# Kernel optimization log

Measured on AMD Instinct MI355X. Metric: run time of the kernel, lower is better.

## Reference

```python
import jax, jax.numpy as jnp
import numpy as np

IN_CHANNELS = 192
BAND_DIM = IN_CHANNELS // 3   # 64
HEADS = 4
HEAD_DIM = BAND_DIM // HEADS  # 16
SCALE = HEAD_DIM ** -0.5


def setup_inputs() -> dict:
    key = jax.random.key(0)
    k1, k2, k3 = jax.random.split(key, 3)
    B, H, W = 8, 128, 128
    hf = jax.random.normal(k1, (B, IN_CHANNELS, H, W), dtype=jnp.float32)
    # torch Linear weights, stored as (in, out) for direct matmul
    W_qkv = jax.random.normal(k2, (BAND_DIM, 3 * BAND_DIM), dtype=jnp.float32) * (BAND_DIM ** -0.5)
    W_proj = jax.random.normal(k3, (BAND_DIM, BAND_DIM), dtype=jnp.float32) * (BAND_DIM ** -0.5)
    b_proj = jnp.zeros((BAND_DIM,), dtype=jnp.float32)
    res_scale = jnp.float32(0.5)
    return {"hf": hf, "W_qkv": W_qkv, "W_proj": W_proj, "b_proj": b_proj, "res_scale": res_scale}


def reference(hf, W_qkv, W_proj, b_proj, res_scale):
    B, Ctot, H, W = hf.shape
    bd, h, hd = BAND_DIM, HEADS, HEAD_DIM
    # (B, 3, bd, H, W) -> (B, H, W, 3, bd) -> (N, 3, bd)
    x = hf.reshape(B, 3, bd, H, W).transpose(0, 3, 4, 1, 2).reshape(-1, 3, bd)
    qkv = x @ W_qkv                                   # (N, 3, 3*bd)
    q, k, v = jnp.split(qkv, 3, axis=-1)
    # (N, 3, bd) -> (N, heads, 3, hd)
    def split_heads(t):
        return t.reshape(-1, 3, h, hd).transpose(0, 2, 1, 3)
    q, k, v = split_heads(q), split_heads(k), split_heads(v)
    attn = jnp.einsum('nhqd,nhkd->nhqk', q, k) * SCALE  # (N, heads, 3, 3)
    attn = jax.nn.softmax(attn, axis=-1)
    y = jnp.einsum('nhqk,nhkd->nhqd', attn, v)          # (N, heads, 3, hd)
    y = y.transpose(0, 2, 1, 3).reshape(-1, 3, bd)      # (N, 3, bd)
    y = y @ W_proj + b_proj
    # (N, 3, bd) -> (B, H, W, 3, bd) -> (B, Ctot, H, W)
    y = y.reshape(B, H, W, 3, bd).transpose(0, 3, 4, 1, 2).reshape(B, Ctot, H, W)
    return hf + res_scale * y
```

## Files before the change

### kernel.cpp

```cpp
#include <hip/hip_runtime.h>


typedef __attribute__((ext_vector_type(8))) short bf16x8;
typedef __attribute__((ext_vector_type(4))) float f32x4;

constexpr int kHW = 16384;
constexpr int kC = 192;

__device__ __forceinline__ unsigned short f2bf(float f) {
  unsigned int u = __float_as_uint(f);
  return (unsigned short)((u + 0x7fffu + ((u >> 16) & 1u)) >> 16);
}

__global__ void pack_weights(const float* __restrict__ Wqkv,
                             const float* __restrict__ Wproj,
                             unsigned char* __restrict__ wsc) {
  const int tid = threadIdx.x;
  const int wid = tid >> 6;
  const int l = tid & 63;
  const int c = l & 15;
  const int g = l >> 4;
  for (int f = wid; f < 24; f += 4) {
    const int m = f >> 1, s = f & 1;
    const int row = m * 16 + c;
    const int k0 = s * 32 + g * 8;
    bf16x8 wf;
#pragma unroll
    for (int j = 0; j < 8; ++j) wf[j] = (short)f2bf(Wqkv[(k0 + j) * 192 + row]);
    *(bf16x8*)(wsc + f * 1024 + l * 16) = wf;
  }
  for (int f = wid; f < 8; f += 4) {
    const int m = f >> 1, s = f & 1;
    const int row = m * 16 + c;
    const int k0 = s * 32 + g * 8;
    bf16x8 wf;
#pragma unroll
    for (int j = 0; j < 8; ++j) wf[j] = (short)f2bf(Wproj[(k0 + j) * 64 + row]);
    *(bf16x8*)(wsc + 24576 + f * 1024 + l * 16) = wf;
  }
}

__global__ __launch_bounds__(256, 4) void hfattn_mfma2(
    const float* __restrict__ hf,
    const unsigned char* __restrict__ wfr,
    const float* __restrict__ bproj,
    const float* __restrict__ rscale,
    float* __restrict__ out) {
  __shared__ char smem[24576];

  const int tid = threadIdx.x;
  const int wid = tid >> 6;
  const int l = tid & 63;
  const int c = l & 15;
  const int g = l >> 4;

  char* const yBase = smem + wid * 6144;
  const f32x4 zz = {0.f, 0.f, 0.f, 0.f};

  const int pxB = blockIdx.x * 64 + wid * 16;
  const int b8 = pxB >> 14;
  const int blkBase = b8 * (kC * kHW);
  const int hw = (pxB & (kHW - 1)) + c;

  float bias_[4][4];
#pragma unroll
  for (int m = 0; m < 4; ++m)
#pragma unroll
    for (int j = 0; j < 4; ++j) bias_[m][j] = bproj[m * 16 + g * 4 + j];
  const float rv = rscale[0];

  bf16x8 Xf[3][2];
#pragma unroll
  for (int b = 0; b < 3; ++b)
#pragma unroll
    for (int s = 0; s < 2; ++s) {
      const int ch0 = b * 64 + s * 32 + g * 8;
      float xr[8];
#pragma unroll
      for (int j = 0; j < 8; ++j) xr[j] = hf[blkBase + (ch0 + j) * kHW + hw];
      bf16x8 xf;
#pragma unroll
      for (int j = 0; j < 8; ++j) xf[j] = (short)f2bf(xr[j]);
      Xf[b][s] = xf;
    }

#pragma unroll 1
  for (int h = 0; h < 4; ++h) {
    const bf16x8 qA0 = *(const bf16x8*)(wfr + (h * 2 + 0) * 1024 + l * 16);
    const bf16x8 qA1 = *(const bf16x8*)(wfr + (h * 2 + 1) * 1024 + l * 16);
    const bf16x8 kA0 = *(const bf16x8*)(wfr + ((4 + h) * 2 + 0) * 1024 + l * 16);
    const bf16x8 kA1 = *(const bf16x8*)(wfr + ((4 + h) * 2 + 1) * 1024 + l * 16);
    f32x4 q[3], k[3];
#pragma unroll
    for (int b = 0; b < 3; ++b) {
      q[b] = __builtin_amdgcn_mfma_f32_16x16x32_bf16(qA0, Xf[b][0], zz, 0, 0, 0);
      q[b] = __builtin_amdgcn_mfma_f32_16x16x32_bf16(qA1, Xf[b][1], q[b], 0, 0, 0);
      k[b] = __builtin_amdgcn_mfma_f32_16x16x32_bf16(kA0, Xf[b][0], zz, 0, 0, 0);
      k[b] = __builtin_amdgcn_mfma_f32_16x16x32_bf16(kA1, Xf[b][1], k[b], 0, 0, 0);
    }
    float P[3][3];
#pragma unroll
    for (int r1 = 0; r1 < 3; ++r1) {
      float sc[3];
#pragma unroll
      for (int r2 = 0; r2 < 3; ++r2) {
        float d = q[r1][0] * k[r2][0] + q[r1][1] * k[r2][1] +
                  q[r1][2] * k[r2][2] + q[r1][3] * k[r2][3];
        d += __shfl_xor(d, 16);
        d += __shfl_xor(d, 32);
        sc[r2] = d * 0.25f;
      }
      const float mx = fmaxf(sc[0], fmaxf(sc[1], sc[2]));
      const float e0 = __expf(sc[0] - mx);
      const float e1 = __expf(sc[1] - mx);
      const float e2 = __expf(sc[2] - mx);
      const float inv = 1.f / (e0 + e1 + e2);
      P[r1][0] = e0 * inv;
      P[r1][1] = e1 * inv;
      P[r1][2] = e2 * inv;
    }
    const bf16x8 vA0 = *(const bf16x8*)(wfr + ((8 + h) * 2 + 0) * 1024 + l * 16);
    const bf16x8 vA1 = *(const bf16x8*)(wfr + ((8 + h) * 2 + 1) * 1024 + l * 16);
    f32x4 v[3];
#pragma unroll
    for (int b = 0; b < 3; ++b) {
      v[b] = __builtin_amdgcn_mfma_f32_16x16x32_bf16(vA0, Xf[b][0], zz, 0, 0, 0);
      v[b] = __builtin_amdgcn_mfma_f32_16x16x32_bf16(vA1, Xf[b][1], v[b], 0, 0, 0);
    }
    const int sp = h >> 1;
    const int gp = (h & 1) * 2 + (g >> 1);
    const int wslot = (gp * 16 + c) * 16 + (g & 1) * 8;
#pragma unroll
    for (int r1 = 0; r1 < 3; ++r1) {
      float y0 = P[r1][0] * v[0][0] + P[r1][1] * v[1][0] + P[r1][2] * v[2][0];
      float y1 = P[r1][0] * v[0][1] + P[r1][1] * v[1][1] + P[r1][2] * v[2][1];
      float y2 = P[r1][0] * v[0][2] + P[r1][1] * v[1][2] + P[r1][2] * v[2][2];
      float y3 = P[r1][0] * v[0][3] + P[r1][1] * v[1][3] + P[r1][2] * v[2][3];
      uint2 pk;
      pk.x = (unsigned)f2bf(y0) | ((unsigned)f2bf(y1) << 16);
      pk.y = (unsigned)f2bf(y2) | ((unsigned)f2bf(y3) << 16);
      *(uint2*)(yBase + (r1 * 2 + sp) * 1024 + wslot) = pk;
    }
  }

#pragma unroll
  for (int b = 0; b < 3; ++b) {
    const bf16x8 yB0 = *(bf16x8*)(yBase + (b * 2 + 0) * 1024 + l * 16);
    const bf16x8 yB1 = *(bf16x8*)(yBase + (b * 2 + 1) * 1024 + l * 16);
#pragma unroll
    for (int m = 0; m < 4; ++m) {
      const bf16x8 pA0 =
          *(const bf16x8*)(wfr + 24576 + (m * 2 + 0) * 1024 + l * 16);
      const bf16x8 pA1 =
          *(const bf16x8*)(wfr + 24576 + (m * 2 + 1) * 1024 + l * 16);
      f32x4 o = __builtin_amdgcn_mfma_f32_16x16x32_bf16(pA0, yB0, zz, 0, 0, 0);
      o = __builtin_amdgcn_mfma_f32_16x16x32_bf16(pA1, yB1, o, 0, 0, 0);
#pragma unroll
      for (int j = 0; j < 4; ++j) {
        const int ch = b * 64 + m * 16 + g * 4 + j;
        const int a = blkBase + ch * kHW + hw;
        out[a] = hf[a] + rv * (o[j] + bias_[m][j]);
      }
    }
  }
}

extern "C" void kernel_launch(void* const* d_in, const int* in_sizes, int n_in,
                              void* d_out, int out_size, void* d_ws,
                              size_t ws_size, hipStream_t stream) {
  const float* hf = (const float*)d_in[0];
  const float* Wqkv = (const float*)d_in[1];
  const float* Wproj = (const float*)d_in[2];
  const float* bproj = (const float*)d_in[3];
  const float* rscale = (const float*)d_in[4];
  float* out = (float*)d_out;
  unsigned char* wsc = (unsigned char*)d_ws;

  hipLaunchKernelGGL(pack_weights, dim3(1), dim3(256), 0, stream, Wqkv, Wproj,
                     wsc);

  const int npix = in_sizes[0] / kC;
  const int nblocks = npix / 64;
  hipLaunchKernelGGL(hfattn_mfma2, dim3(nblocks), dim3(256), 0, stream, hf, wsc,
                     bproj, rscale, out);
}
```

Before: 60.40 us.

## Replace LDS staging of attention output with cross-lane shuffles and unroll heads

The attention output is no longer staged in shared memory. The per-head outputs are moved into the projection MFMA B-operand layout using wave shuffles, and the head loop is fully unrolled through templates with sched barriers. The residual hf reads are batched ahead of the projection MFMAs, and the bias is loaded as float4. This removes the LDS round-trip and 24KB of shared memory per block, which could raise occupancy. In exchange it adds many shuffle instructions and more register pressure from the unrolled heads.

```diff
diff --git a/kernel.cpp b/kernel.cpp
--- a/kernel.cpp
+++ b/kernel.cpp
@@ -40,33 +40,109 @@
   }
 }
 
-__global__ __launch_bounds__(256, 4) void hfattn_mfma2(
+template <int H>
+__device__ __forceinline__ void head_compute(const bf16x8* __restrict__ wp,
+                                             int l, const bf16x8 (&Xf)[3][2],
+                                             uint2 (&pk)[3]) {
+  const f32x4 zz = {0.f, 0.f, 0.f, 0.f};
+  const bf16x8 qA0 = wp[(H * 2 + 0) * 64 + l];
+  const bf16x8 qA1 = wp[(H * 2 + 1) * 64 + l];
+  const bf16x8 kA0 = wp[((4 + H) * 2 + 0) * 64 + l];
+  const bf16x8 kA1 = wp[((4 + H) * 2 + 1) * 64 + l];
+  f32x4 q[3], k[3];
+#pragma unroll
+  for (int b = 0; b < 3; ++b) {
+    q[b] = __builtin_amdgcn_mfma_f32_16x16x32_bf16(qA0, Xf[b][0], zz, 0, 0, 0);
+    q[b] = __builtin_amdgcn_mfma_f32_16x16x32_bf16(qA1, Xf[b][1], q[b], 0, 0, 0);
+    k[b] = __builtin_amdgcn_mfma_f32_16x16x32_bf16(kA0, Xf[b][0], zz, 0, 0, 0);
+    k[b] = __builtin_amdgcn_mfma_f32_16x16x32_bf16(kA1, Xf[b][1], k[b], 0, 0, 0);
+  }
+  float P[3][3];
+#pragma unroll
+  for (int r1 = 0; r1 < 3; ++r1) {
+    float sc[3];
+#pragma unroll
+    for (int r2 = 0; r2 < 3; ++r2) {
+      float d = q[r1][0] * k[r2][0] + q[r1][1] * k[r2][1] +
+                q[r1][2] * k[r2][2] + q[r1][3] * k[r2][3];
+      d += __shfl_xor(d, 16);
+      d += __shfl_xor(d, 32);
+      sc[r2] = d * 0.25f;
+    }
+    const float mx = fmaxf(sc[0], fmaxf(sc[1], sc[2]));
+    const float e0 = __expf(sc[0] - mx);
+    const float e1 = __expf(sc[1] - mx);
+    const float e2 = __expf(sc[2] - mx);
+    const float inv = 1.f / (e0 + e1 + e2);
+    P[r1][0] = e0 * inv;
+    P[r1][1] = e1 * inv;
+    P[r1][2] = e2 * inv;
+  }
+  const bf16x8 vA0 = wp[((8 + H) * 2 + 0) * 64 + l];
+  const bf16x8 vA1 = wp[((8 + H) * 2 + 1) * 64 + l];
+  f32x4 v[3];
+#pragma unroll
+  for (int b = 0; b < 3; ++b) {
+    v[b] = __builtin_amdgcn_mfma_f32_16x16x32_bf16(vA0, Xf[b][0], zz, 0, 0, 0);
+    v[b] = __builtin_amdgcn_mfma_f32_16x16x32_bf16(vA1, Xf[b][1], v[b], 0, 0, 0);
+  }
+#pragma unroll
+  for (int r1 = 0; r1 < 3; ++r1) {
+    f32x4 y = P[r1][0] * v[0] + P[r1][1] * v[1] + P[r1][2] * v[2];
+    uint2 p;
+    p.x = (unsigned)f2bf(y[0]) | ((unsigned)f2bf(y[1]) << 16);
+    p.y = (unsigned)f2bf(y[2]) | ((unsigned)f2bf(y[3]) << 16);
+    pk[r1] = p;
+  }
+}
+
+__device__ __forceinline__ bf16x8 build_frag(uint2 pkA, uint2 pkB, int srcA,
+                                             bool hi) {
+  uint2 a0, a1, b0, b1;
+  a0.x = (unsigned)__shfl((int)pkA.x, srcA, 64);
+  a0.y = (unsigned)__shfl((int)pkA.y, srcA, 64);
+  a1.x = (unsigned)__shfl((int)pkB.x, srcA, 64);
+  a1.y = (unsigned)__shfl((int)pkB.y, srcA, 64);
+  const int srcB = srcA + 16;
+  b0.x = (unsigned)__shfl((int)pkA.x, srcB, 64);
+  b0.y = (unsigned)__shfl((int)pkA.y, srcB, 64);
+  b1.x = (unsigned)__shfl((int)pkB.x, srcB, 64);
+  b1.y = (unsigned)__shfl((int)pkB.y, srcB, 64);
+  const uint2 lo = hi ? a1 : a0;
+  const uint2 hi2 = hi ? b1 : b0;
+  union {
+    unsigned u[4];
+    bf16x8 v;
+  } r;
+  r.u[0] = lo.x;
+  r.u[1] = lo.y;
+  r.u[2] = hi2.x;
+  r.u[3] = hi2.y;
+  return r.v;
+}
+
+__global__ __launch_bounds__(256, 4) void hfattn_mfma4(
     const float* __restrict__ hf,
     const unsigned char* __restrict__ wfr,
     const float* __restrict__ bproj,
     const float* __restrict__ rscale,
     float* __restrict__ out) {
-  __shared__ char smem[24576];
-
   const int tid = threadIdx.x;
   const int wid = tid >> 6;
   const int l = tid & 63;
   const int c = l & 15;
   const int g = l >> 4;
 
-  char* const yBase = smem + wid * 6144;
   const f32x4 zz = {0.f, 0.f, 0.f, 0.f};
+  const bf16x8* const wp = (const bf16x8*)wfr;
 
   const int pxB = blockIdx.x * 64 + wid * 16;
   const int b8 = pxB >> 14;
   const int blkBase = b8 * (kC * kHW);
   const int hw = (pxB & (kHW - 1)) + c;
-
-  float bias_[4][4];
-#pragma unroll
-  for (int m = 0; m < 4; ++m)
-#pragma unroll
-    for (int j = 0; j < 4; ++j) bias_[m][j] = bproj[m * 16 + g * 4 + j];
+  const float* __restrict__ hfp = hf + blkBase + hw;
+  float* __restrict__ outp = out + blkBase + hw;
+
   const float rv = rscale[0];
 
   bf16x8 Xf[3][2];
@@ -77,89 +153,62 @@
       const int ch0 = b * 64 + s * 32 + g * 8;
       float xr[8];
 #pragma unroll
-      for (int j = 0; j < 8; ++j) xr[j] = hf[blkBase + (ch0 + j) * kHW + hw];
+      for (int j = 0; j < 8; ++j) xr[j] = hfp[(ch0 + j) * kHW];
       bf16x8 xf;
 #pragma unroll
       for (int j = 0; j < 8; ++j) xf[j] = (short)f2bf(xr[j]);
       Xf[b][s] = xf;
     }
 
-#pragma unroll 1
-  for (int h = 0; h < 4; ++h) {
-    const bf16x8 qA0 = *(const bf16x8*)(wfr + (h * 2 + 0) * 1024 + l * 16);
-    const bf16x8 qA1 = *(const bf16x8*)(wfr + (h * 2 + 1) * 1024 + l * 16);
-    const bf16x8 kA0 = *(const bf16x8*)(wfr + ((4 + h) * 2 + 0) * 1024 + l * 16);
-    const bf16x8 kA1 = *(const bf16x8*)(wfr + ((4 + h) * 2 + 1) * 1024 + l * 16);
-    f32x4 q[3], k[3];
-#pragma unroll
-    for (int b = 0; b < 3; ++b) {
-      q[b] = __builtin_amdgcn_mfma_f32_16x16x32_bf16(qA0, Xf[b][0], zz, 0, 0, 0);
-      q[b] = __builtin_amdgcn_mfma_f32_16x16x32_bf16(qA1, Xf[b][1], q[b], 0, 0, 0);
-      k[b] = __builtin_amdgcn_mfma_f32_16x16x32_bf16(kA0, Xf[b][0], zz, 0, 0, 0);
-      k[b] = __builtin_amdgcn_mfma_f32_16x16x32_bf16(kA1, Xf[b][1], k[b], 0, 0, 0);
-    }
-    float P[3][3];
-#pragma unroll
-    for (int r1 = 0; r1 < 3; ++r1) {
-      float sc[3];
-#pragma unroll
-      for (int r2 = 0; r2 < 3; ++r2) {
-        float d = q[r1][0] * k[r2][0] + q[r1][1] * k[r2][1] +
-                  q[r1][2] * k[r2][2] + q[r1][3] * k[r2][3];
-        d += __shfl_xor(d, 16);
-        d += __shfl_xor(d, 32);
-        sc[r2] = d * 0.25f;
-      }
-      const float mx = fmaxf(sc[0], fmaxf(sc[1], sc[2]));
-      const float e0 = __expf(sc[0] - mx);
-      const float e1 = __expf(sc[1] - mx);
-      const float e2 = __expf(sc[2] - mx);
-      const float inv = 1.f / (e0 + e1 + e2);
-      P[r1][0] = e0 * inv;
-      P[r1][1] = e1 * inv;
-      P[r1][2] = e2 * inv;
-    }
-    const bf16x8 vA0 = *(const bf16x8*)(wfr + ((8 + h) * 2 + 0) * 1024 + l * 16);
-    const bf16x8 vA1 = *(const bf16x8*)(wfr + ((8 + h) * 2 + 1) * 1024 + l * 16);
-    f32x4 v[3];
-#pragma unroll
-    for (int b = 0; b < 3; ++b) {
-      v[b] = __builtin_amdgcn_mfma_f32_16x16x32_bf16(vA0, Xf[b][0], zz, 0, 0, 0);
-      v[b] = __builtin_amdgcn_mfma_f32_16x16x32_bf16(vA1, Xf[b][1], v[b], 0, 0, 0);
-    }
-    const int sp = h >> 1;
-    const int gp = (h & 1) * 2 + (g >> 1);
-    const int wslot = (gp * 16 + c) * 16 + (g & 1) * 8;
-#pragma unroll
-    for (int r1 = 0; r1 < 3; ++r1) {
-      float y0 = P[r1][0] * v[0][0] + P[r1][1] * v[1][0] + P[r1][2] * v[2][0];
-      float y1 = P[r1][0] * v[0][1] + P[r1][1] * v[1][1] + P[r1][2] * v[2][1];
-      float y2 = P[r1][0] * v[0][2] + P[r1][1] * v[1][2] + P[r1][2] * v[2][2];
-      float y3 = P[r1][0] * v[0][3] + P[r1][1] * v[1][3] + P[r1][2] * v[2][3];
-      uint2 pk;
-      pk.x = (unsigned)f2bf(y0) | ((unsigned)f2bf(y1) << 16);
-      pk.y = (unsigned)f2bf(y2) | ((unsigned)f2bf(y3) << 16);
-      *(uint2*)(yBase + (r1 * 2 + sp) * 1024 + wslot) = pk;
-    }
+  const int srcA = ((g & 1) * 2) * 16 + c;
+  const bool hi = (g >> 1) & 1;
+
+  uint2 pkA[3], pkB[3];
+  bf16x8 yS0[3], yS1[3];
+
+  head_compute<0>(wp, l, Xf, pkA);
+  __builtin_amdgcn_sched_barrier(0);
+  head_compute<1>(wp, l, Xf, pkB);
+  __builtin_amdgcn_sched_barrier(0);
+#pragma unroll
+  for (int b = 0; b < 3; ++b) yS0[b] = build_frag(pkA[b], pkB[b], srcA, hi);
+  __builtin_amdgcn_sched_barrier(0);
+  head_compute<2>(wp, l, Xf, pkA);
+  __builtin_amdgcn_sched_barrier(0);
+  head_compute<3>(wp, l, Xf, pkB);
+  __builtin_amdgcn_sched_barrier(0);
+#pragma unroll
+  for (int b = 0; b < 3; ++b) yS1[b] = build_frag(pkA[b], pkB[b], srcA, hi);
+
+  float bias_[4][4];
+#pragma unroll
+  for (int m = 0; m < 4; ++m) {
+    const float4 bj = *(const float4*)(bproj + m * 16 + g * 4);
+    bias_[m][0] = bj.x;
+    bias_[m][1] = bj.y;
+    bias_[m][2] = bj.z;
+    bias_[m][3] = bj.w;
   }
 
 #pragma unroll
   for (int b = 0; b < 3; ++b) {
-    const bf16x8 yB0 = *(bf16x8*)(yBase + (b * 2 + 0) * 1024 + l * 16);
-    const bf16x8 yB1 = *(bf16x8*)(yBase + (b * 2 + 1) * 1024 + l * 16);
+    float res[4][4];
+#pragma unroll
+    for (int m = 0; m < 4; ++m)
+#pragma unroll
+      for (int j = 0; j < 4; ++j)
+        res[m][j] = hfp[(b * 64 + m * 16 + g * 4 + j) * kHW];
 #pragma unroll
     for (int m = 0; m < 4; ++m) {
-      const bf16x8 pA0 =
-          *(const bf16x8*)(wfr + 24576 + (m * 2 + 0) * 1024 + l * 16);
-      const bf16x8 pA1 =
-          *(const bf16x8*)(wfr + 24576 + (m * 2 + 1) * 1024 + l * 16);
-      f32x4 o = __builtin_amdgcn_mfma_f32_16x16x32_bf16(pA0, yB0, zz, 0, 0, 0);
-      o = __builtin_amdgcn_mfma_f32_16x16x32_bf16(pA1, yB1, o, 0, 0, 0);
+      const bf16x8 pA0 = wp[(24 + m * 2 + 0) * 64 + l];
+      const bf16x8 pA1 = wp[(24 + m * 2 + 1) * 64 + l];
+      f32x4 o =
+          __builtin_amdgcn_mfma_f32_16x16x32_bf16(pA0, yS0[b], zz, 0, 0, 0);
+      o = __builtin_amdgcn_mfma_f32_16x16x32_bf16(pA1, yS1[b], o, 0, 0, 0);
 #pragma unroll
       for (int j = 0; j < 4; ++j) {
-        const int ch = b * 64 + m * 16 + g * 4 + j;
-        const int a = blkBase + ch * kHW + hw;
-        out[a] = hf[a] + rv * (o[j] + bias_[m][j]);
+        outp[(b * 64 + m * 16 + g * 4 + j) * kHW] =
+            fmaf(rv, o[j] + bias_[m][j], res[m][j]);
       }
     }
   }
@@ -181,6 +230,6 @@
 
   const int npix = in_sizes[0] / kC;
   const int nblocks = npix / 64;
-  hipLaunchKernelGGL(hfattn_mfma2, dim3(nblocks), dim3(256), 0, stream, hf, wsc,
+  hipLaunchKernelGGL(hfattn_mfma4, dim3(nblocks), dim3(256), 0, stream, hf, wsc,
                      bproj, rscale, out);
 }
```

Result: slower. 71.13 us (+17.8%).
